# Kernel tuning notes

Hardware: AMD Instinct MI355X
Metric: run time of the kernel (lower is better)

Reference implementation:

```python
import jax, jax.numpy as jnp
import numpy as np

B, S, D, H = 4, 2048, 1024, 16
DK = D // H  # 64


def setup_inputs() -> dict:
    key = jax.random.key(0)
    ks = jax.random.split(key, 12)
    sc = 0.02
    return {
        "q": jax.random.normal(ks[0], (B, S, D), jnp.float32),
        "k": jax.random.normal(ks[1], (B, S, D), jnp.float32),
        "v": jax.random.normal(ks[2], (B, S, D), jnp.float32),
        "mask": jax.random.randint(ks[3], (B, S, S), 0, 2).astype(bool),
        "Wq": jax.random.normal(ks[4], (H, D, DK), jnp.float32) * sc,
        "bq": jax.random.normal(ks[5], (H, DK), jnp.float32) * sc,
        "Wk": jax.random.normal(ks[6], (H, D, DK), jnp.float32) * sc,
        "bk": jax.random.normal(ks[7], (H, DK), jnp.float32) * sc,
        "Wv": jax.random.normal(ks[8], (H, D, DK), jnp.float32) * sc,
        "bv": jax.random.normal(ks[9], (H, DK), jnp.float32) * sc,
        "Wo": jax.random.normal(ks[10], (D, D), jnp.float32) * sc,
        "bo": jax.random.normal(ks[11], (D,), jnp.float32) * sc,
    }


def reference(q, k, v, mask, Wq, bq, Wk, bk, Wv, bv, Wo, bo):
    # per-head projections, batched over heads: [b,s,d] x [h,d,k] -> [b,h,s,k]
    qh = jnp.einsum('bsd,hdk->bhsk', q, Wq) + bq[None, :, None, :]
    kh = jnp.einsum('bsd,hdk->bhsk', k, Wk) + bk[None, :, None, :]
    vh = jnp.einsum('bsd,hdk->bhsk', v, Wv) + bv[None, :, None, :]
    dk = qh.shape[-1]
    scores = jnp.einsum('bhsk,bhtk->bhst', qh, kh) / (dk ** 0.5)
    # original uses masked_fill(mask == False, -1e-06) -- NOT -inf; keep faithful
    scores = jnp.where(mask[:, None, :, :], scores, jnp.float32(-1e-06))
    attn = jax.nn.softmax(scores, axis=-1)
    out = jnp.einsum('bhst,bhtk->bhsk', attn, vh)
    b, h, s, _ = out.shape
    out = out.transpose(0, 2, 1, 3).reshape(b, s, h * dk)  # concat heads
    return out @ Wo + bo
```

## Files before the change

kernel.cpp:

```cpp
#include <hip/hip_runtime.h>
#include <stdint.h>

#define Bn 4
#define Sn 2048
#define Dn 1024
#define Hn 16
#define DKn 64

typedef __bf16 bf16x8 __attribute__((ext_vector_type(8)));
typedef float f32x4 __attribute__((ext_vector_type(4)));
typedef unsigned short u16;
typedef unsigned long long u64;

union ABFrag { bf16x8 v; uint4 u; };
union V8 { u16 us[8]; uint4 u; };

__device__ __forceinline__ u16 f2bf(float f) {
  union { float f; uint32_t u; } a; a.f = f;
  return (u16)((a.u + 0x7fffu + ((a.u >> 16) & 1u)) >> 16);
}

__device__ __forceinline__ void gload16(const void* g, void* l) {
  __builtin_amdgcn_global_load_lds((const __attribute__((address_space(1))) unsigned int*)g,
                                   (__attribute__((address_space(3))) unsigned int*)l, 16, 0, 0);
}

__device__ __forceinline__ f32x4 zero4() { f32x4 z; z[0]=0.f; z[1]=0.f; z[2]=0.f; z[3]=0.f; return z; }


__global__ void conv_bf16_all(const float* __restrict__ q, const float* __restrict__ k,
                              const float* __restrict__ v, u16* __restrict__ dq,
                              u16* __restrict__ dk, u16* __restrict__ dv) {
  int i = blockIdx.x * 256 + threadIdx.x;
  int seg = i >> 21, j = i & 2097151;
  const float* s = (seg == 0) ? q : (seg == 1) ? k : v;
  u16* d = (seg == 0) ? dq : (seg == 1) ? dk : dv;
  float4 vv = ((const float4*)s)[j];
  V8 o;
  o.us[0] = f2bf(vv.x); o.us[1] = f2bf(vv.y); o.us[2] = f2bf(vv.z); o.us[3] = f2bf(vv.w);
  ((uint2*)d)[j] = make_uint2(o.u.x, o.u.y);
}

__device__ __forceinline__ void tile_tr_body(const float* __restrict__ s, int ss,
                                             u16* __restrict__ d, int ds) {
  __shared__ float t[64 * 65];
  int tid = threadIdx.x;
  int r = tid >> 2, c0 = (tid & 3) * 16;
  #pragma unroll
  for (int j = 0; j < 4; ++j) {
    float4 v = *(const float4*)(s + r * ss + c0 + j * 4);
    t[(c0 + j * 4 + 0) * 65 + r] = v.x;
    t[(c0 + j * 4 + 1) * 65 + r] = v.y;
    t[(c0 + j * 4 + 2) * 65 + r] = v.z;
    t[(c0 + j * 4 + 3) * 65 + r] = v.w;
  }
  __syncthreads();
  V8 o0, o1;
  #pragma unroll
  for (int j = 0; j < 8; ++j) o0.us[j] = f2bf(t[r * 65 + c0 + j]);
  #pragma unroll
  for (int j = 0; j < 8; ++j) o1.us[j] = f2bf(t[r * 65 + c0 + 8 + j]);
  *(uint4*)(d + r * ds + c0) = o0.u;
  *(uint4*)(d + r * ds + c0 + 8) = o1.u;
}

__global__ void prep_w_all(const float* __restrict__ Wq, const float* __restrict__ Wk,
                           const float* __restrict__ Wv, const float* __restrict__ Wo,
                           u16* __restrict__ wcatt, u16* __restrict__ wot) {
  int bid = blockIdx.x;
  if (bid < 768) {
    int w = bid >> 8, h = (bid >> 4) & 15, db = bid & 15;
    const float* src = (w == 0) ? Wq : (w == 1) ? Wk : Wv;
    tile_tr_body(src + (h * 1024 + db * 64) * 64, 64,
                 wcatt + (size_t)(w * 1024 + h * 64) * 1024 + db * 64, 1024);
  } else {
    int b2 = bid - 768;
    int rb = b2 >> 4, cb = b2 & 15;
    tile_tr_body(Wo + (size_t)rb * 64 * 1024 + cb * 64, 1024,
                 wot + (size_t)cb * 64 * 1024 + rb * 64, 1024);
  }
}

__global__ void mask_detect(const uint32_t* __restrict__ mw, int* __restrict__ flag) {
  int t = threadIdx.x;
  uint32_t acc = 0;
  for (int j = 0; j < 4; ++j) acc |= (mw[t * 4 + j] > 1u) ? 1u : 0u;
  unsigned long long bal = __ballot(acc != 0);
  __shared__ int s[4];
  if ((t & 63) == 0) s[t >> 6] = (bal != 0ull) ? 1 : 0;
  __syncthreads();
  if (t == 0) *flag = s[0] | s[1] | s[2] | s[3];
}

__global__ void mask_pack(const void* __restrict__ mraw, const int* __restrict__ flag,
                          u64* __restrict__ mb, int nwords) {
  int i = blockIdx.x * 256 + threadIdx.x;
  if (i >= nwords) return;
  u64 w = 0;
  if (*flag) {
    const uchar4* p = (const uchar4*)mraw + (size_t)i * 16;
    #pragma unroll
    for (int j = 0; j < 16; ++j) {
      uchar4 v = p[j];
      w |= ((u64)(v.x != 0)) << (j * 4 + 0);
      w |= ((u64)(v.y != 0)) << (j * 4 + 1);
      w |= ((u64)(v.z != 0)) << (j * 4 + 2);
      w |= ((u64)(v.w != 0)) << (j * 4 + 3);
    }
  } else {
    const uint4* p = (const uint4*)mraw + (size_t)i * 16;
    #pragma unroll
    for (int j = 0; j < 16; ++j) {
      uint4 v = p[j];
      w |= ((u64)(v.x != 0)) << (j * 4 + 0);
      w |= ((u64)(v.y != 0)) << (j * 4 + 1);
      w |= ((u64)(v.z != 0)) << (j * 4 + 2);
      w |= ((u64)(v.w != 0)) << (j * 4 + 3);
    }
  }
  mb[i] = w;
}

template<int MODE>
__launch_bounds__(256)
__global__ void gemm_kernel(const u16* __restrict__ Aq, const u16* __restrict__ Ak,
                            const u16* __restrict__ Av, const u16* __restrict__ Bm,
                            const float* __restrict__ bq, const float* __restrict__ bk,
                            const float* __restrict__ bv,
                            u16* __restrict__ Oq, u16* __restrict__ Ok, u16* __restrict__ Ov,
                            float* __restrict__ Of) {
  __shared__ char lds[32768];
  char* Al = lds;
  char* Bl = lds + 16384;
  const int tid = threadIdx.x, w = tid >> 6, lane = tid & 63;
  const int n0 = blockIdx.x * 128, m0 = blockIdx.y * 128;
  int which = 0;
  const u16* A = Aq;
  if (MODE == 0) { which = n0 >> 10; A = (which == 0) ? Aq : (which == 1) ? Ak : Av; }

  f32x4 acc[2][8];
  #pragma unroll
  for (int i = 0; i < 2; ++i)
    #pragma unroll
    for (int j = 0; j < 8; ++j) acc[i][j] = zero4();

  for (int kt = 0; kt < 16; ++kt) {
    __syncthreads();
    #pragma unroll
    for (int si = 0; si < 4; ++si) {
      int c = si * 256 + tid, r = c >> 3, cb = c & 7;
      gload16((const char*)A + (((size_t)(m0 + r)) << 11) + (size_t)(kt * 128) + ((cb ^ (r & 7)) << 4),
              Al + si * 4096 + w * 1024);
    }
    #pragma unroll
    for (int si = 0; si < 4; ++si) {
      int c = si * 256 + tid, r = c >> 3, cb = c & 7;
      gload16((const char*)Bm + (((size_t)(n0 + r)) << 11) + (size_t)(kt * 128) + ((cb ^ (r & 7)) << 4),
              Bl + si * 4096 + w * 1024);
    }
    __syncthreads();
    #pragma unroll
    for (int kk = 0; kk < 2; ++kk) {
      ABFrag a0, a1;
      {
        int row = w * 32 + (lane & 15);
        int ch = (lane >> 4) + kk * 4;
        a0.u = *(const uint4*)(Al + row * 128 + ((ch ^ (row & 7)) << 4));
        row += 16;
        a1.u = *(const uint4*)(Al + row * 128 + ((ch ^ (row & 7)) << 4));
      }
      #pragma unroll
      for (int nn = 0; nn < 8; ++nn) {
        int row = nn * 16 + (lane & 15);
        int ch = (lane >> 4) + kk * 4;
        ABFrag bb; bb.u = *(const uint4*)(Bl + row * 128 + ((ch ^ (row & 7)) << 4));
        acc[0][nn] = __builtin_amdgcn_mfma_f32_16x16x32_bf16(a0.v, bb.v, acc[0][nn], 0, 0, 0);
        acc[1][nn] = __builtin_amdgcn_mfma_f32_16x16x32_bf16(a1.v, bb.v, acc[1][nn], 0, 0, 0);
      }
    }
  }

  if (MODE == 0) {
    const float esc = (which == 0) ? 0.18033688011112042f : 1.0f;
    const float* bias = (which == 0) ? bq : (which == 1) ? bk : bv;
    #pragma unroll
    for (int nn = 0; nn < 8; ++nn) {
      int ng = (n0 & 1023) + nn * 16 + (lane & 15);
      int h = ng >> 6, dk = ng & 63;
      float bsv = bias[ng];
      #pragma unroll
      for (int mm = 0; mm < 2; ++mm) {
        #pragma unroll
        for (int r = 0; r < 4; ++r) {
          int mg = m0 + w * 32 + mm * 16 + (lane >> 4) * 4 + r;
          int b = mg >> 11, s = mg & 2047;
          float val = (acc[mm][nn][r] + bsv) * esc;
          if (which == 2) {
            Ov[(((size_t)((b * Hn + h) * DKn + dk)) << 11) + s] = f2bf(val);
          } else {
            u16* O = (which == 0) ? Oq : Ok;
            O[(((size_t)(b * Hn + h)) * Sn + s) * DKn + dk] = f2bf(val);
          }
        }
      }
    }
  } else {
    #pragma unroll
    for (int nn = 0; nn < 8; ++nn) {
      int ng = n0 + nn * 16 + (lane & 15);
      float bsv = bq[ng];
      #pragma unroll
      for (int mm = 0; mm < 2; ++mm) {
        #pragma unroll
        for (int r = 0; r < 4; ++r) {
          int mg = m0 + w * 32 + mm * 16 + (lane >> 4) * 4 + r;
          Of[(size_t)mg * 1024 + ng] = acc[mm][nn][r] + bsv;
        }
      }
    }
  }
}

__launch_bounds__(256, 4)
__global__ void flash_attn(const u16* __restrict__ qh, const u16* __restrict__ kh,
                           const u16* __restrict__ vt, const u64* __restrict__ mb,
                           u16* __restrict__ o) {
  __shared__ char lds[40960];
  const int tid = threadIdx.x, w = tid >> 6, lane = tid & 63;
  const int l15 = lane & 15, g = lane >> 4;
  char* Plds = lds + 32768 + w * 2048;

  int bid = blockIdx.x;
  int wg = (bid & 7) * 256 + (bid >> 3);
  const int bh = wg >> 5, b = bh >> 4, h = bh & 15;
  const int qr = (wg & 31) * 64 + w * 16;

  ABFrag aq0, aq1;
  {
    const char* qrow = (const char*)(qh + ((size_t)bh * Sn + qr + l15) * DKn);
    aq0.u = *(const uint4*)(qrow + g * 16);
    aq1.u = *(const uint4*)(qrow + 64 + g * 16);
  }

  const char* kbase = (const char*)(kh + (size_t)bh * Sn * DKn);
  const char* vbase = (const char*)(vt + (size_t)bh * DKn * Sn);
  const int rowg = qr + g * 4;
  const char* mp = (const char*)mb + ((size_t)b * Sn + rowg) * 256;

  f32x4 oacc[4];
  float psum[4];
  #pragma unroll
  for (int nn = 0; nn < 4; ++nn) oacc[nn] = zero4();
  #pragma unroll
  for (int r = 0; r < 4; ++r) psum[r] = 0.f;

  const int r0 = tid >> 3, cb0 = tid & 7;
  const int sr = (256 + tid) >> 3, scb = (256 + tid) & 7;
  const int pw_base = (g * 4) * 128;
  const int pr_base = l15 * 128;
  const int pr_sw   = (l15 & 7) << 4;

  gload16(kbase + (size_t)r0 * 128 + ((cb0 ^ (r0 & 7)) << 4), lds + w * 1024);
  gload16(kbase + (size_t)sr * 128 + ((scb ^ (sr & 7)) << 4), lds + 4096 + w * 1024);
  gload16(vbase + (size_t)r0 * (Sn * 2) + ((cb0 ^ (r0 & 7)) << 4), lds + 8192 + w * 1024);
  gload16(vbase + (size_t)sr * (Sn * 2) + ((scb ^ (sr & 7)) << 4), lds + 12288 + w * 1024);

  for (int kt = 0; kt < Sn / 64; ++kt) {
    char* bufK = lds + (kt & 1) * 16384;
    char* bufV = bufK + 8192;
    char* nK = lds + ((kt & 1) ^ 1) * 16384;
    char* nV = nK + 8192;

    u64 mw0 = *(const u64*)(mp + kt * 8);
    u64 mw1 = *(const u64*)(mp + kt * 8 + 256);
    u64 mw2 = *(const u64*)(mp + kt * 8 + 512);
    u64 mw3 = *(const u64*)(mp + kt * 8 + 768);

    asm volatile("s_waitcnt lgkmcnt(0)" ::: "memory");
    __builtin_amdgcn_sched_barrier(0);
    __builtin_amdgcn_s_barrier();
    __builtin_amdgcn_sched_barrier(0);

    if (kt < Sn / 64 - 1) {
      gload16(kbase + (size_t)((kt + 1) * 64 + r0) * 128 + ((cb0 ^ (r0 & 7)) << 4), nK + w * 1024);
      gload16(kbase + (size_t)((kt + 1) * 64 + sr) * 128 + ((scb ^ (sr & 7)) << 4), nK + 4096 + w * 1024);
      gload16(vbase + (size_t)r0 * (Sn * 2) + (size_t)((kt + 1) * 128) + ((cb0 ^ (r0 & 7)) << 4), nV + w * 1024);
      gload16(vbase + (size_t)sr * (Sn * 2) + (size_t)((kt + 1) * 128) + ((scb ^ (sr & 7)) << 4), nV + 4096 + w * 1024);
      __builtin_amdgcn_sched_barrier(0);
      asm volatile("s_waitcnt vmcnt(8)" ::: "memory");
    } else {
      __builtin_amdgcn_sched_barrier(0);
      asm volatile("s_waitcnt vmcnt(4)" ::: "memory");
    }
    __builtin_amdgcn_sched_barrier(0);
    __builtin_amdgcn_s_barrier();
    __builtin_amdgcn_sched_barrier(0);

    f32x4 sacc[4];
    #pragma unroll
    for (int nn = 0; nn < 4; ++nn) sacc[nn] = zero4();
    #pragma unroll
    for (int kk = 0; kk < 2; ++kk) {
      ABFrag aq = (kk == 0) ? aq0 : aq1;
      #pragma unroll
      for (int nn = 0; nn < 4; ++nn) {
        int row = nn * 16 + l15;
        int ch = g + kk * 4;
        ABFrag kf; kf.u = *(const uint4*)(bufK + row * 128 + ((ch ^ (row & 7)) << 4));
        sacc[nn] = __builtin_amdgcn_mfma_f32_16x16x32_bf16(aq.v, kf.v, sacc[nn], 0, 0, 0);
      }
    }

    #pragma unroll
    for (int r = 0; r < 4; ++r) {
      u64 mwr = (r == 0) ? mw0 : (r == 1) ? mw1 : (r == 2) ? mw2 : mw3;
      int prow = pw_base + r * 128;
      int psw = (((g * 4 + r) & 7) << 4);
      #pragma unroll
      for (int nn = 0; nn < 4; ++nn) {
        float pe = __builtin_amdgcn_exp2f(sacc[nn][r]);
        unsigned m16 = (unsigned)(mwr >> (nn * 16)) & 0xffffu;
        float pv = ((m16 >> l15) & 1u) ? pe : 1.0f;
        psum[r] += pv;
        *(__bf16*)(Plds + prow + (((nn * 32) + l15 * 2) ^ psw)) = (__bf16)pv;
      }
    }

    #pragma unroll
    for (int kk = 0; kk < 2; ++kk) {
      ABFrag pa;
      pa.u = *(const uint4*)(Plds + pr_base + ((kk * 64 + g * 16) ^ pr_sw));
      #pragma unroll
      for (int nn = 0; nn < 4; ++nn) {
        int row = nn * 16 + l15;
        int ch = g + kk * 4;
        ABFrag vb; vb.u = *(const uint4*)(bufV + row * 128 + ((ch ^ (row & 7)) << 4));
        oacc[nn] = __builtin_amdgcn_mfma_f32_16x16x32_bf16(pa.v, vb.v, oacc[nn], 0, 0, 0);
      }
    }
  }

  #pragma unroll
  for (int r = 0; r < 4; ++r) {
    float s = psum[r];
    s += __shfl_xor(s, 1, 16);
    s += __shfl_xor(s, 2, 16);
    s += __shfl_xor(s, 4, 16);
    s += __shfl_xor(s, 8, 16);
    float inv = 1.f / s;
    int sg = qr + g * 4 + r;
    #pragma unroll
    for (int nn = 0; nn < 4; ++nn) {
      int col = h * 64 + nn * 16 + l15;
      o[((size_t)(b * Sn) + sg) * Dn + col] = f2bf(oacc[nn][r] * inv);
    }
  }
}


extern "C" void kernel_launch(void* const* d_in, const int* in_sizes, int n_in,
                              void* d_out, int out_size, void* d_ws, size_t ws_size,
                              hipStream_t stream) {
  (void)in_sizes; (void)n_in; (void)out_size; (void)ws_size;
  const float* q  = (const float*)d_in[0];
  const float* k  = (const float*)d_in[1];
  const float* v  = (const float*)d_in[2];
  const void*  mask = d_in[3];
  const float* Wq = (const float*)d_in[4];
  const float* bq = (const float*)d_in[5];
  const float* Wk = (const float*)d_in[6];
  const float* bk = (const float*)d_in[7];
  const float* Wv = (const float*)d_in[8];
  const float* bv = (const float*)d_in[9];
  const float* Wo = (const float*)d_in[10];
  const float* bo = (const float*)d_in[11];
  float* out = (float*)d_out;

  char* ws = (char*)d_ws;
  const size_t SZ = (size_t)8192 * 1024 * 2;
  u16* qbf   = (u16*)(ws);
  u16* kbf   = (u16*)(ws + SZ);
  u16* vbf   = (u16*)(ws + 2 * SZ);
  u16* Wcatt = (u16*)(ws + 3 * SZ);
  u16* Wot   = (u16*)(ws + 3 * SZ + 6291456);
  u16* qhp   = (u16*)(ws + 3 * SZ + 8388608);
  u16* khp   = (u16*)((char*)qhp + SZ);
  u16* vtp   = (u16*)((char*)khp + SZ);
  int* flag  = (int*)((char*)vtp + SZ);

  conv_bf16_all<<<24576, 256, 0, stream>>>(q, k, v, qbf, kbf, vbf);
  prep_w_all<<<1024, 256, 0, stream>>>(Wq, Wk, Wv, Wo, Wcatt, Wot);

  gemm_kernel<0><<<dim3(24, 64), 256, 0, stream>>>(qbf, kbf, vbf, Wcatt, bq, bk, bv,
                                                   qhp, khp, vtp, nullptr);

  mask_detect<<<1, 256, 0, stream>>>((const uint32_t*)mask, flag);
  u64* mbw = (u64*)vbf;
  mask_pack<<<1024, 256, 0, stream>>>(mask, flag, mbw, 262144);

  u16* oc = qbf;
  flash_attn<<<2048, 256, 0, stream>>>(qhp, khp, vtp, mbw, oc);

  gemm_kernel<1><<<dim3(8, 64), 256, 0, stream>>>(oc, nullptr, nullptr, Wot, bo,
                                                  nullptr, nullptr, nullptr,
                                                  nullptr, nullptr, out);
}
```

Baseline: 464.4 us.

## Software-pipeline flash attention: overlap PV of previous tile with QK of current

Restructures the attention loop so the P·V MFMAs for tile t-1 run after the Q·K MFMAs for tile t, with P double-buffered in LDS and V loaded one step later into a separate buffer. The per-row softmax sum now comes from an extra MFMA against a ones vector instead of scalar adds and shuffles, and s_setprio is raised around the MFMA blocks. LDS grows to 48KB and launch bounds drop to 3 blocks per CU, trading occupancy for more overlap between exp/mask work and matrix ops.

```diff
diff --git a/kernel.cpp b/kernel.cpp
--- a/kernel.cpp
+++ b/kernel.cpp
@@ -221,14 +221,13 @@
   }
 }
 
-__launch_bounds__(256, 4)
+__launch_bounds__(256, 3)
 __global__ void flash_attn(const u16* __restrict__ qh, const u16* __restrict__ kh,
                            const u16* __restrict__ vt, const u64* __restrict__ mb,
                            u16* __restrict__ o) {
-  __shared__ char lds[40960];
+  __shared__ char lds[49152];
   const int tid = threadIdx.x, w = tid >> 6, lane = tid & 63;
   const int l15 = lane & 15, g = lane >> 4;
-  char* Plds = lds + 32768 + w * 2048;
 
   int bid = blockIdx.x;
   int wg = (bid & 7) * 256 + (bid >> 3);
@@ -242,17 +241,21 @@
     aq1.u = *(const uint4*)(qrow + 64 + g * 16);
   }
 
+  ABFrag ones;
+  {
+    unsigned ov = (l15 == 0) ? 0x3F803F80u : 0u;
+    ones.u = make_uint4(ov, ov, ov, ov);
+  }
+
   const char* kbase = (const char*)(kh + (size_t)bh * Sn * DKn);
   const char* vbase = (const char*)(vt + (size_t)bh * DKn * Sn);
   const int rowg = qr + g * 4;
   const char* mp = (const char*)mb + ((size_t)b * Sn + rowg) * 256;
 
-  f32x4 oacc[4];
-  float psum[4];
+  f32x4 oacc[4], psacc;
   #pragma unroll
   for (int nn = 0; nn < 4; ++nn) oacc[nn] = zero4();
-  #pragma unroll
-  for (int r = 0; r < 4; ++r) psum[r] = 0.f;
+  psacc = zero4();
 
   const int r0 = tid >> 3, cb0 = tid & 7;
   const int sr = (256 + tid) >> 3, scb = (256 + tid) & 7;
@@ -262,91 +265,132 @@
 
   gload16(kbase + (size_t)r0 * 128 + ((cb0 ^ (r0 & 7)) << 4), lds + w * 1024);
   gload16(kbase + (size_t)sr * 128 + ((scb ^ (sr & 7)) << 4), lds + 4096 + w * 1024);
-  gload16(vbase + (size_t)r0 * (Sn * 2) + ((cb0 ^ (r0 & 7)) << 4), lds + 8192 + w * 1024);
-  gload16(vbase + (size_t)sr * (Sn * 2) + ((scb ^ (sr & 7)) << 4), lds + 12288 + w * 1024);
-
-  for (int kt = 0; kt < Sn / 64; ++kt) {
-    char* bufK = lds + (kt & 1) * 16384;
-    char* bufV = bufK + 8192;
-    char* nK = lds + ((kt & 1) ^ 1) * 16384;
-    char* nV = nK + 8192;
-
-    u64 mw0 = *(const u64*)(mp + kt * 8);
-    u64 mw1 = *(const u64*)(mp + kt * 8 + 256);
-    u64 mw2 = *(const u64*)(mp + kt * 8 + 512);
-    u64 mw3 = *(const u64*)(mp + kt * 8 + 768);
+  gload16(vbase + (size_t)r0 * (Sn * 2) + ((cb0 ^ (r0 & 7)) << 4), lds + 16384 + w * 1024);
+  gload16(vbase + (size_t)sr * (Sn * 2) + ((scb ^ (sr & 7)) << 4), lds + 20480 + w * 1024);
+
+  for (int t = 0; t < 32; ++t) {
+    const int p = t & 1;
+    char* Kb    = lds + p * 8192;
+    char* Kn    = lds + (p ^ 1) * 8192;
+    char* Vprev = lds + 16384 + (p ^ 1) * 8192;
+    char* Pc    = lds + 32768 + p * 8192 + w * 2048;
+    char* Pp    = lds + 32768 + (p ^ 1) * 8192 + w * 2048;
+
+    if (t < 31) {
+      gload16(kbase + (size_t)((t + 1) * 64 + r0) * 128 + ((cb0 ^ (r0 & 7)) << 4), Kn + w * 1024);
+      gload16(kbase + (size_t)((t + 1) * 64 + sr) * 128 + ((scb ^ (sr & 7)) << 4), Kn + 4096 + w * 1024);
+      __builtin_amdgcn_sched_barrier(0);
+      asm volatile("s_waitcnt vmcnt(4)" ::: "memory");
+    } else {
+      __builtin_amdgcn_sched_barrier(0);
+      asm volatile("s_waitcnt vmcnt(2)" ::: "memory");
+    }
+    __builtin_amdgcn_sched_barrier(0);
+    __builtin_amdgcn_s_barrier();
+    __builtin_amdgcn_sched_barrier(0);
+
+    u64 mw0 = *(const u64*)(mp + t * 8);
+    u64 mw1 = *(const u64*)(mp + t * 8 + 256);
+    u64 mw2 = *(const u64*)(mp + t * 8 + 512);
+    u64 mw3 = *(const u64*)(mp + t * 8 + 768);
+
+    f32x4 sacc[4];
+    #pragma unroll
+    for (int nn = 0; nn < 4; ++nn) sacc[nn] = zero4();
+    __builtin_amdgcn_s_setprio(1);
+    #pragma unroll
+    for (int kk = 0; kk < 2; ++kk) {
+      ABFrag aq = (kk == 0) ? aq0 : aq1;
+      #pragma unroll
+      for (int nn = 0; nn < 4; ++nn) {
+        int row = nn * 16 + l15;
+        int ch = g + kk * 4;
+        ABFrag kf; kf.u = *(const uint4*)(Kb + row * 128 + ((ch ^ (row & 7)) << 4));
+        sacc[nn] = __builtin_amdgcn_mfma_f32_16x16x32_bf16(aq.v, kf.v, sacc[nn], 0, 0, 0);
+      }
+    }
+    __builtin_amdgcn_s_setprio(0);
+
+    if (t > 0) {
+      ABFrag pa0, pa1;
+      pa0.u = *(const uint4*)(Pp + pr_base + ((g * 16) ^ pr_sw));
+      pa1.u = *(const uint4*)(Pp + pr_base + ((64 + g * 16) ^ pr_sw));
+      __builtin_amdgcn_s_setprio(1);
+      #pragma unroll
+      for (int kk = 0; kk < 2; ++kk) {
+        ABFrag pa = (kk == 0) ? pa0 : pa1;
+        #pragma unroll
+        for (int nn = 0; nn < 4; ++nn) {
+          int row = nn * 16 + l15;
+          int ch = g + kk * 4;
+          ABFrag vb; vb.u = *(const uint4*)(Vprev + row * 128 + ((ch ^ (row & 7)) << 4));
+          oacc[nn] = __builtin_amdgcn_mfma_f32_16x16x32_bf16(pa.v, vb.v, oacc[nn], 0, 0, 0);
+        }
+        psacc = __builtin_amdgcn_mfma_f32_16x16x32_bf16(pa.v, ones.v, psacc, 0, 0, 0);
+      }
+      __builtin_amdgcn_s_setprio(0);
+    }
+
+    #pragma unroll
+    for (int r = 0; r < 4; ++r) {
+      u64 mwr = (r == 0) ? mw0 : (r == 1) ? mw1 : (r == 2) ? mw2 : mw3;
+      unsigned sa = ((unsigned)mwr) >> l15;
+      unsigned sb = ((unsigned)(mwr >> 32)) >> l15;
+      int prow = pw_base + r * 128;
+      int psw = (((g * 4 + r) & 7) << 4);
+      float pe0 = __builtin_amdgcn_exp2f(sacc[0][r]);
+      float pe1 = __builtin_amdgcn_exp2f(sacc[1][r]);
+      float pe2 = __builtin_amdgcn_exp2f(sacc[2][r]);
+      float pe3 = __builtin_amdgcn_exp2f(sacc[3][r]);
+      float pv0 = (sa & 1u) ? pe0 : 1.0f;
+      float pv1 = (sa & 0x10000u) ? pe1 : 1.0f;
+      float pv2 = (sb & 1u) ? pe2 : 1.0f;
+      float pv3 = (sb & 0x10000u) ? pe3 : 1.0f;
+      *(__bf16*)(Pc + prow + ((l15 * 2 +  0) ^ psw)) = (__bf16)pv0;
+      *(__bf16*)(Pc + prow + ((l15 * 2 + 32) ^ psw)) = (__bf16)pv1;
+      *(__bf16*)(Pc + prow + ((l15 * 2 + 64) ^ psw)) = (__bf16)pv2;
+      *(__bf16*)(Pc + prow + ((l15 * 2 + 96) ^ psw)) = (__bf16)pv3;
+    }
 
     asm volatile("s_waitcnt lgkmcnt(0)" ::: "memory");
     __builtin_amdgcn_sched_barrier(0);
     __builtin_amdgcn_s_barrier();
     __builtin_amdgcn_sched_barrier(0);
-
-    if (kt < Sn / 64 - 1) {
-      gload16(kbase + (size_t)((kt + 1) * 64 + r0) * 128 + ((cb0 ^ (r0 & 7)) << 4), nK + w * 1024);
-      gload16(kbase + (size_t)((kt + 1) * 64 + sr) * 128 + ((scb ^ (sr & 7)) << 4), nK + 4096 + w * 1024);
-      gload16(vbase + (size_t)r0 * (Sn * 2) + (size_t)((kt + 1) * 128) + ((cb0 ^ (r0 & 7)) << 4), nV + w * 1024);
-      gload16(vbase + (size_t)sr * (Sn * 2) + (size_t)((kt + 1) * 128) + ((scb ^ (sr & 7)) << 4), nV + 4096 + w * 1024);
-      __builtin_amdgcn_sched_barrier(0);
-      asm volatile("s_waitcnt vmcnt(8)" ::: "memory");
-    } else {
-      __builtin_amdgcn_sched_barrier(0);
-      asm volatile("s_waitcnt vmcnt(4)" ::: "memory");
-    }
-    __builtin_amdgcn_sched_barrier(0);
-    __builtin_amdgcn_s_barrier();
-    __builtin_amdgcn_sched_barrier(0);
-
-    f32x4 sacc[4];
-    #pragma unroll
-    for (int nn = 0; nn < 4; ++nn) sacc[nn] = zero4();
+    if (t < 31) {
+      gload16(vbase + (size_t)r0 * (Sn * 2) + (size_t)((t + 1) * 128) + ((cb0 ^ (r0 & 7)) << 4),
+              Vprev + w * 1024);
+      gload16(vbase + (size_t)sr * (Sn * 2) + (size_t)((t + 1) * 128) + ((scb ^ (sr & 7)) << 4),
+              Vprev + 4096 + w * 1024);
+    }
+  }
+
+  asm volatile("s_waitcnt vmcnt(0)" ::: "memory");
+  __builtin_amdgcn_sched_barrier(0);
+  __builtin_amdgcn_s_barrier();
+  __builtin_amdgcn_sched_barrier(0);
+  {
+    char* Pe = lds + 32768 + 8192 + w * 2048;
+    char* Ve = lds + 16384 + 8192;
+    ABFrag pa0, pa1;
+    pa0.u = *(const uint4*)(Pe + pr_base + ((g * 16) ^ pr_sw));
+    pa1.u = *(const uint4*)(Pe + pr_base + ((64 + g * 16) ^ pr_sw));
     #pragma unroll
     for (int kk = 0; kk < 2; ++kk) {
-      ABFrag aq = (kk == 0) ? aq0 : aq1;
+      ABFrag pa = (kk == 0) ? pa0 : pa1;
       #pragma unroll
       for (int nn = 0; nn < 4; ++nn) {
         int row = nn * 16 + l15;
         int ch = g + kk * 4;
-        ABFrag kf; kf.u = *(const uint4*)(bufK + row * 128 + ((ch ^ (row & 7)) << 4));
-        sacc[nn] = __builtin_amdgcn_mfma_f32_16x16x32_bf16(aq.v, kf.v, sacc[nn], 0, 0, 0);
-      }
-    }
-
-    #pragma unroll
-    for (int r = 0; r < 4; ++r) {
-      u64 mwr = (r == 0) ? mw0 : (r == 1) ? mw1 : (r == 2) ? mw2 : mw3;
-      int prow = pw_base + r * 128;
-      int psw = (((g * 4 + r) & 7) << 4);
-      #pragma unroll
-      for (int nn = 0; nn < 4; ++nn) {
-        float pe = __builtin_amdgcn_exp2f(sacc[nn][r]);
-        unsigned m16 = (unsigned)(mwr >> (nn * 16)) & 0xffffu;
-        float pv = ((m16 >> l15) & 1u) ? pe : 1.0f;
-        psum[r] += pv;
-        *(__bf16*)(Plds + prow + (((nn * 32) + l15 * 2) ^ psw)) = (__bf16)pv;
-      }
-    }
-
-    #pragma unroll
-    for (int kk = 0; kk < 2; ++kk) {
-      ABFrag pa;
-      pa.u = *(const uint4*)(Plds + pr_base + ((kk * 64 + g * 16) ^ pr_sw));
-      #pragma unroll
-      for (int nn = 0; nn < 4; ++nn) {
-        int row = nn * 16 + l15;
-        int ch = g + kk * 4;
-        ABFrag vb; vb.u = *(const uint4*)(bufV + row * 128 + ((ch ^ (row & 7)) << 4));
+        ABFrag vb; vb.u = *(const uint4*)(Ve + row * 128 + ((ch ^ (row & 7)) << 4));
         oacc[nn] = __builtin_amdgcn_mfma_f32_16x16x32_bf16(pa.v, vb.v, oacc[nn], 0, 0, 0);
       }
+      psacc = __builtin_amdgcn_mfma_f32_16x16x32_bf16(pa.v, ones.v, psacc, 0, 0, 0);
     }
   }
 
   #pragma unroll
   for (int r = 0; r < 4; ++r) {
-    float s = psum[r];
-    s += __shfl_xor(s, 1, 16);
-    s += __shfl_xor(s, 2, 16);
-    s += __shfl_xor(s, 4, 16);
-    s += __shfl_xor(s, 8, 16);
+    float s = __shfl(psacc[r], lane & 48, 64);
     float inv = 1.f / s;
     int sg = qr + g * 4 + r;
     #pragma unroll
```

Result: no change. 468.0 us (+0.8%).

## Process 32 query rows per wave in flash attention, sum rows via MFMA

Applied to the files above, without the earlier changes.

Each wave now handles two 16-row query blocks (128 rows per workgroup, half the grid), so every K/V tile loaded into LDS is reused twice. The K/V double buffer is replaced by a single buffer with plain __syncthreads around the loads. Row sums of P now come from an extra MFMA against a ones vector instead of VALU adds and shuffles. s_setprio is raised around the PV MFMAs. This trades K/V loads and VALU work for more registers and no prefetch overlap, which could lower occupancy and expose memory latency.

```diff
diff --git a/kernel.cpp b/kernel.cpp
--- a/kernel.cpp
+++ b/kernel.cpp
@@ -225,134 +225,128 @@
 __global__ void flash_attn(const u16* __restrict__ qh, const u16* __restrict__ kh,
                            const u16* __restrict__ vt, const u64* __restrict__ mb,
                            u16* __restrict__ o) {
-  __shared__ char lds[40960];
+  __shared__ char lds[32768];
+  char* Klds = lds;
+  char* Vlds = lds + 8192;
   const int tid = threadIdx.x, w = tid >> 6, lane = tid & 63;
   const int l15 = lane & 15, g = lane >> 4;
-  char* Plds = lds + 32768 + w * 2048;
+  char* Plds = lds + 16384 + w * 4096;
 
   int bid = blockIdx.x;
-  int wg = (bid & 7) * 256 + (bid >> 3);
-  const int bh = wg >> 5, b = bh >> 4, h = bh & 15;
-  const int qr = (wg & 31) * 64 + w * 16;
-
-  ABFrag aq0, aq1;
+  int wg = (bid & 7) * 128 + (bid >> 3);
+  const int bh = wg >> 4, b = bh >> 4, h = bh & 15;
+  const int qr = (wg & 15) * 128 + w * 32;
+
+  ABFrag aq[2][2];
+  #pragma unroll
+  for (int rb = 0; rb < 2; ++rb) {
+    const char* qrow = (const char*)(qh + ((size_t)bh * Sn + qr + rb * 16 + l15) * DKn);
+    aq[rb][0].u = *(const uint4*)(qrow + g * 16);
+    aq[rb][1].u = *(const uint4*)(qrow + 64 + g * 16);
+  }
+
+  ABFrag ones;
   {
-    const char* qrow = (const char*)(qh + ((size_t)bh * Sn + qr + l15) * DKn);
-    aq0.u = *(const uint4*)(qrow + g * 16);
-    aq1.u = *(const uint4*)(qrow + 64 + g * 16);
+    unsigned ov = (l15 == 0) ? 0x3F803F80u : 0u;
+    ones.u = make_uint4(ov, ov, ov, ov);
   }
 
   const char* kbase = (const char*)(kh + (size_t)bh * Sn * DKn);
   const char* vbase = (const char*)(vt + (size_t)bh * DKn * Sn);
-  const int rowg = qr + g * 4;
-  const char* mp = (const char*)mb + ((size_t)b * Sn + rowg) * 256;
-
-  f32x4 oacc[4];
-  float psum[4];
-  #pragma unroll
-  for (int nn = 0; nn < 4; ++nn) oacc[nn] = zero4();
-  #pragma unroll
-  for (int r = 0; r < 4; ++r) psum[r] = 0.f;
+  const char* mp0 = (const char*)mb + ((size_t)b * Sn + qr + g * 4) * 256;
+  const char* mp1 = mp0 + 16 * 256;
+
+  f32x4 oacc[2][4], psacc[2];
+  #pragma unroll
+  for (int rb = 0; rb < 2; ++rb) {
+    #pragma unroll
+    for (int nn = 0; nn < 4; ++nn) oacc[rb][nn] = zero4();
+    psacc[rb] = zero4();
+  }
 
   const int r0 = tid >> 3, cb0 = tid & 7;
   const int sr = (256 + tid) >> 3, scb = (256 + tid) & 7;
-  const int pw_base = (g * 4) * 128;
-  const int pr_base = l15 * 128;
-  const int pr_sw   = (l15 & 7) << 4;
-
-  gload16(kbase + (size_t)r0 * 128 + ((cb0 ^ (r0 & 7)) << 4), lds + w * 1024);
-  gload16(kbase + (size_t)sr * 128 + ((scb ^ (sr & 7)) << 4), lds + 4096 + w * 1024);
-  gload16(vbase + (size_t)r0 * (Sn * 2) + ((cb0 ^ (r0 & 7)) << 4), lds + 8192 + w * 1024);
-  gload16(vbase + (size_t)sr * (Sn * 2) + ((scb ^ (sr & 7)) << 4), lds + 12288 + w * 1024);
-
-  for (int kt = 0; kt < Sn / 64; ++kt) {
-    char* bufK = lds + (kt & 1) * 16384;
-    char* bufV = bufK + 8192;
-    char* nK = lds + ((kt & 1) ^ 1) * 16384;
-    char* nV = nK + 8192;
-
-    u64 mw0 = *(const u64*)(mp + kt * 8);
-    u64 mw1 = *(const u64*)(mp + kt * 8 + 256);
-    u64 mw2 = *(const u64*)(mp + kt * 8 + 512);
-    u64 mw3 = *(const u64*)(mp + kt * 8 + 768);
-
-    asm volatile("s_waitcnt lgkmcnt(0)" ::: "memory");
-    __builtin_amdgcn_sched_barrier(0);
-    __builtin_amdgcn_s_barrier();
-    __builtin_amdgcn_sched_barrier(0);
-
-    if (kt < Sn / 64 - 1) {
-      gload16(kbase + (size_t)((kt + 1) * 64 + r0) * 128 + ((cb0 ^ (r0 & 7)) << 4), nK + w * 1024);
-      gload16(kbase + (size_t)((kt + 1) * 64 + sr) * 128 + ((scb ^ (sr & 7)) << 4), nK + 4096 + w * 1024);
-      gload16(vbase + (size_t)r0 * (Sn * 2) + (size_t)((kt + 1) * 128) + ((cb0 ^ (r0 & 7)) << 4), nV + w * 1024);
-      gload16(vbase + (size_t)sr * (Sn * 2) + (size_t)((kt + 1) * 128) + ((scb ^ (sr & 7)) << 4), nV + 4096 + w * 1024);
-      __builtin_amdgcn_sched_barrier(0);
-      asm volatile("s_waitcnt vmcnt(8)" ::: "memory");
-    } else {
-      __builtin_amdgcn_sched_barrier(0);
-      asm volatile("s_waitcnt vmcnt(4)" ::: "memory");
-    }
-    __builtin_amdgcn_sched_barrier(0);
-    __builtin_amdgcn_s_barrier();
-    __builtin_amdgcn_sched_barrier(0);
-
-    f32x4 sacc[4];
-    #pragma unroll
-    for (int nn = 0; nn < 4; ++nn) sacc[nn] = zero4();
+  const int pr_sw = (l15 & 7) << 4;
+
+  for (int t = 0; t < 32; ++t) {
+    __syncthreads();
+    gload16(kbase + (size_t)(t * 64 + r0) * 128 + ((cb0 ^ (r0 & 7)) << 4), Klds + w * 1024);
+    gload16(kbase + (size_t)(t * 64 + sr) * 128 + ((scb ^ (sr & 7)) << 4), Klds + 4096 + w * 1024);
+    gload16(vbase + (size_t)r0 * (Sn * 2) + (size_t)(t * 128) + ((cb0 ^ (r0 & 7)) << 4), Vlds + w * 1024);
+    gload16(vbase + (size_t)sr * (Sn * 2) + (size_t)(t * 128) + ((scb ^ (sr & 7)) << 4), Vlds + 4096 + w * 1024);
+    u64 m0[4], m1[4];
+    #pragma unroll
+    for (int r = 0; r < 4; ++r) {
+      m0[r] = *(const u64*)(mp0 + r * 256 + t * 8);
+      m1[r] = *(const u64*)(mp1 + r * 256 + t * 8);
+    }
+    __syncthreads();
+
+    unsigned lo0[4], hi0[4], lo1[4], hi1[4];
+    #pragma unroll
+    for (int r = 0; r < 4; ++r) {
+      lo0[r] = ((unsigned)m0[r]) >> l15;  hi0[r] = ((unsigned)(m0[r] >> 32)) >> l15;
+      lo1[r] = ((unsigned)m1[r]) >> l15;  hi1[r] = ((unsigned)(m1[r] >> 32)) >> l15;
+    }
+
+    #pragma unroll
+    for (int nn = 0; nn < 4; ++nn) {
+      int krow = nn * 16 + l15;
+      ABFrag kf0, kf1;
+      kf0.u = *(const uint4*)(Klds + krow * 128 + ((g ^ (krow & 7)) << 4));
+      kf1.u = *(const uint4*)(Klds + krow * 128 + (((g + 4) ^ (krow & 7)) << 4));
+      f32x4 s0 = zero4(), s1 = zero4();
+      s0 = __builtin_amdgcn_mfma_f32_16x16x32_bf16(aq[0][0].v, kf0.v, s0, 0, 0, 0);
+      s0 = __builtin_amdgcn_mfma_f32_16x16x32_bf16(aq[0][1].v, kf1.v, s0, 0, 0, 0);
+      s1 = __builtin_amdgcn_mfma_f32_16x16x32_bf16(aq[1][0].v, kf0.v, s1, 0, 0, 0);
+      s1 = __builtin_amdgcn_mfma_f32_16x16x32_bf16(aq[1][1].v, kf1.v, s1, 0, 0, 0);
+      unsigned mbit = (nn & 1) ? 0x10000u : 1u;
+      #pragma unroll
+      for (int r = 0; r < 4; ++r) {
+        unsigned w0 = (nn < 2) ? lo0[r] : hi0[r];
+        unsigned w1 = (nn < 2) ? lo1[r] : hi1[r];
+        float pe0 = __builtin_amdgcn_exp2f(s0[r]);
+        float pe1 = __builtin_amdgcn_exp2f(s1[r]);
+        float pv0 = (w0 & mbit) ? pe0 : 1.0f;
+        float pv1 = (w1 & mbit) ? pe1 : 1.0f;
+        int row0 = g * 4 + r;
+        int row1 = 16 + g * 4 + r;
+        *(__bf16*)(Plds + row0 * 128 + ((nn * 32 + l15 * 2) ^ ((row0 & 7) << 4))) = (__bf16)pv0;
+        *(__bf16*)(Plds + row1 * 128 + ((nn * 32 + l15 * 2) ^ ((row1 & 7) << 4))) = (__bf16)pv1;
+      }
+    }
+
+    __builtin_amdgcn_s_setprio(1);
     #pragma unroll
     for (int kk = 0; kk < 2; ++kk) {
-      ABFrag aq = (kk == 0) ? aq0 : aq1;
+      ABFrag pa0, pa1;
+      pa0.u = *(const uint4*)(Plds + l15 * 128 + ((kk * 64 + g * 16) ^ pr_sw));
+      pa1.u = *(const uint4*)(Plds + (16 + l15) * 128 + ((kk * 64 + g * 16) ^ pr_sw));
       #pragma unroll
       for (int nn = 0; nn < 4; ++nn) {
-        int row = nn * 16 + l15;
-        int ch = g + kk * 4;
-        ABFrag kf; kf.u = *(const uint4*)(bufK + row * 128 + ((ch ^ (row & 7)) << 4));
-        sacc[nn] = __builtin_amdgcn_mfma_f32_16x16x32_bf16(aq.v, kf.v, sacc[nn], 0, 0, 0);
-      }
-    }
-
+        int vrow = nn * 16 + l15;
+        ABFrag vb; vb.u = *(const uint4*)(Vlds + vrow * 128 + (((g + kk * 4) ^ (vrow & 7)) << 4));
+        oacc[0][nn] = __builtin_amdgcn_mfma_f32_16x16x32_bf16(pa0.v, vb.v, oacc[0][nn], 0, 0, 0);
+        oacc[1][nn] = __builtin_amdgcn_mfma_f32_16x16x32_bf16(pa1.v, vb.v, oacc[1][nn], 0, 0, 0);
+      }
+      psacc[0] = __builtin_amdgcn_mfma_f32_16x16x32_bf16(pa0.v, ones.v, psacc[0], 0, 0, 0);
+      psacc[1] = __builtin_amdgcn_mfma_f32_16x16x32_bf16(pa1.v, ones.v, psacc[1], 0, 0, 0);
+    }
+    __builtin_amdgcn_s_setprio(0);
+  }
+
+  #pragma unroll
+  for (int rb = 0; rb < 2; ++rb) {
     #pragma unroll
     for (int r = 0; r < 4; ++r) {
-      u64 mwr = (r == 0) ? mw0 : (r == 1) ? mw1 : (r == 2) ? mw2 : mw3;
-      int prow = pw_base + r * 128;
-      int psw = (((g * 4 + r) & 7) << 4);
+      float s = __shfl(psacc[rb][r], lane & 48, 64);
+      float inv = 1.f / s;
+      int sg = qr + rb * 16 + g * 4 + r;
       #pragma unroll
       for (int nn = 0; nn < 4; ++nn) {
-        float pe = __builtin_amdgcn_exp2f(sacc[nn][r]);
-        unsigned m16 = (unsigned)(mwr >> (nn * 16)) & 0xffffu;
-        float pv = ((m16 >> l15) & 1u) ? pe : 1.0f;
-        psum[r] += pv;
-        *(__bf16*)(Plds + prow + (((nn * 32) + l15 * 2) ^ psw)) = (__bf16)pv;
-      }
-    }
-
-    #pragma unroll
-    for (int kk = 0; kk < 2; ++kk) {
-      ABFrag pa;
-      pa.u = *(const uint4*)(Plds + pr_base + ((kk * 64 + g * 16) ^ pr_sw));
-      #pragma unroll
-      for (int nn = 0; nn < 4; ++nn) {
-        int row = nn * 16 + l15;
-        int ch = g + kk * 4;
-        ABFrag vb; vb.u = *(const uint4*)(bufV + row * 128 + ((ch ^ (row & 7)) << 4));
-        oacc[nn] = __builtin_amdgcn_mfma_f32_16x16x32_bf16(pa.v, vb.v, oacc[nn], 0, 0, 0);
-      }
-    }
-  }
-
-  #pragma unroll
-  for (int r = 0; r < 4; ++r) {
-    float s = psum[r];
-    s += __shfl_xor(s, 1, 16);
-    s += __shfl_xor(s, 2, 16);
-    s += __shfl_xor(s, 4, 16);
-    s += __shfl_xor(s, 8, 16);
-    float inv = 1.f / s;
-    int sg = qr + g * 4 + r;
-    #pragma unroll
-    for (int nn = 0; nn < 4; ++nn) {
-      int col = h * 64 + nn * 16 + l15;
-      o[((size_t)(b * Sn) + sg) * Dn + col] = f2bf(oacc[nn][r] * inv);
+        int col = h * 64 + nn * 16 + l15;
+        o[((size_t)(b * Sn) + sg) * Dn + col] = f2bf(oacc[rb][nn][r] * inv);
+      }
     }
   }
 }
@@ -399,7 +393,7 @@
   mask_pack<<<1024, 256, 0, stream>>>(mask, flag, mbw, 262144);
 
   u16* oc = qbf;
-  flash_attn<<<2048, 256, 0, stream>>>(qhp, khp, vtp, mbw, oc);
+  flash_attn<<<1024, 256, 0, stream>>>(qhp, khp, vtp, mbw, oc);
 
   gemm_kernel<1><<<dim3(8, 64), 256, 0, stream>>>(oc, nullptr, nullptr, Wot, bo,
                                                   nullptr, nullptr, nullptr,
```

New measurement: 440.5 us. 5.2% less time.
